# Performance work log

Measured on AMD Instinct MI355X. Metric: run time of the kernel, lower is better.

Reference implementation:

```python
import jax, jax.numpy as jnp
import numpy as np

T, B, IN, H, OUT, K = 1024, 128, 32, 512, 32, 64


def frac_weights(d):
    # d: [H] per-channel fractional differencing order (= 0.5*sigmoid(b_d)).
    # pi_j = pi_{j-1} * (j-1-d)/j, pi_0 = 1 (coeffs of (1-B)^d expansion).
    # Returned layout matches torch get_ws: index 0 -> lag K, index K-1 -> lag 1.
    j = jnp.arange(1, K + 1, dtype=d.dtype)[:, None]          # [K,1]
    pi = jnp.cumprod((j - 1.0 - d[None, :]) / j, axis=0)       # [K,H], pi[j-1]=coeff lag j
    return pi[::-1]                                            # [K,H]


def frac_filter(x, pi):
    # x: [T,B,H]; pi: [K,H] (lag K..1). Computes x_tilde[t] = x[t] + sum_j pi_j x[t-j]
    # (zero history before t=0, matching a zero-initialized memory buffer)
    # via a causal depthwise convolution.
    Hc = pi.shape[1]
    kern = jnp.concatenate([pi, jnp.ones((1, Hc), pi.dtype)], axis=0)  # [K+1,H]
    kern = kern.T[:, None, :]                                          # [H,1,K+1]
    xb = x.transpose(1, 2, 0)                                          # [B,H,T]
    y = jax.lax.conv_general_dilated(
        xb, kern, window_strides=(1,), padding=[(K, 0)],
        dimension_numbers=("NCH", "OIH", "NCH"), feature_group_count=Hc)
    return y.transpose(2, 0, 1)                                        # [T,B,H]


def rnn_layer(x, W_ih, b_ih, W_hh, b_hh, W_ho, b_ho, pi):
    # MRNNFixDCell over full sequence: fractional-differencing filter on the
    # layer input, then tanh RNN recurrence, then linear readout per step.
    xt = frac_filter(x, pi)
    pre = jnp.einsum('tbi,hi->tbh', xt, W_ih) + b_ih + b_hh   # input part precomputed

    def step(h, p):
        h = jnp.tanh(p + h @ W_hh.T)
        return h, h

    h0 = jnp.zeros((x.shape[1], W_hh.shape[0]), x.dtype)
    _, hs = jax.lax.scan(step, h0, pre)                        # [T,B,H]
    return jnp.einsum('tbh,oh->tbo', hs, W_ho) + b_ho          # [T,B,out]


def setup_inputs() -> dict:
    key = jax.random.key(0)
    ks = jax.random.split(key, 10)
    s = 0.05
    return {
        "inputs": jax.random.normal(ks[0], (T, B, IN), jnp.float32),
        "b_d":   jax.random.normal(ks[1], (1, H), jnp.float32) * 0.1,
        "W_emb": jax.random.normal(ks[2], (H, IN), jnp.float32) * s,
        "b_emb": jnp.zeros((H,), jnp.float32),
        "W_ih0": jax.random.normal(ks[3], (H, H), jnp.float32) * s,
        "b_ih0": jnp.zeros((H,), jnp.float32),
        "W_hh0": jax.random.normal(ks[4], (H, H), jnp.float32) * s,
        "b_hh0": jnp.zeros((H,), jnp.float32),
        "W_ho0": jax.random.normal(ks[5], (H, H), jnp.float32) * s,
        "b_ho0": jnp.zeros((H,), jnp.float32),
        "W_ih1": jax.random.normal(ks[6], (H, H), jnp.float32) * s,
        "b_ih1": jnp.zeros((H,), jnp.float32),
        "W_hh1": jax.random.normal(ks[7], (H, H), jnp.float32) * s,
        "b_hh1": jnp.zeros((H,), jnp.float32),
        "W_ho1": jax.random.normal(ks[8], (OUT, H), jnp.float32) * s,
        "b_ho1": jnp.zeros((OUT,), jnp.float32),
    }


def reference(inputs, b_d, W_emb, b_emb,
              W_ih0, b_ih0, W_hh0, b_hh0, W_ho0, b_ho0,
              W_ih1, b_ih1, W_hh1, b_hh1, W_ho1, b_ho1):
    x = jnp.einsum('tbi,hi->tbh', inputs, W_emb) + b_emb       # input embedding
    d = 0.5 * jax.nn.sigmoid(b_d)[0]                           # [H], fixed d per channel
    pi = frac_weights(d)                                       # [K,H]
    y0 = rnn_layer(x,  W_ih0, b_ih0, W_hh0, b_hh0, W_ho0, b_ho0, pi)
    y1 = rnn_layer(y0, W_ih1, b_ih1, W_hh1, b_hh1, W_ho1, b_ho1, pi)
    return y1[-1]                                              # last-step output [B,OUT]
```

## Files before the change

### kernel.cpp

```cpp
#include <hip/hip_runtime.h>
#include <hip/hip_bf16.h>

#define Tn 1024
#define Bn 128
#define INn 32
#define Hn 512
#define OUTn 32
#define Kn 64
#define LPAD 536

typedef __attribute__((ext_vector_type(8))) __bf16 bf16x8;
typedef __attribute__((ext_vector_type(4))) float f32x4;
typedef __attribute__((ext_vector_type(4))) unsigned int u32x4;
typedef __attribute__((ext_vector_type(2))) unsigned int u32x2;

typedef const __attribute__((address_space(1))) void* gas_p;
typedef __attribute__((address_space(3))) void* las_p;

static __device__ __forceinline__ float bf2f(unsigned short u) {
    union { unsigned int i; float f; } c; c.i = ((unsigned int)u) << 16; return c.f;
}
static __device__ __forceinline__ unsigned short f2bf(float f) {
    union { float f; unsigned int i; } c; c.f = f;
    unsigned int x = c.i;
    return (unsigned short)((x + 0x7fffu + ((x >> 16) & 1u)) >> 16);
}
static __device__ __forceinline__ float tanh_fast(float x) {
    float xc = fminf(fmaxf(x, -10.f), 10.f);
    float e = __expf(2.f * xc);
    return (e - 1.f) * __builtin_amdgcn_rcpf(e + 1.f);
}

__global__ __launch_bounds__(256) void cvt_k(const float* __restrict__ in,
                                             unsigned short* __restrict__ out, int n4) {
    int i = blockIdx.x * 256 + threadIdx.x;
    if (i < n4) {
        float4 v = ((const float4*)in)[i];
        ushort4 o;
        o.x = f2bf(v.x); o.y = f2bf(v.y); o.z = f2bf(v.z); o.w = f2bf(v.w);
        ((ushort4*)out)[i] = o;
    }
}

__global__ __launch_bounds__(512) void prep_small(const float* __restrict__ b_d,
                                                  const float* __restrict__ bih0, const float* __restrict__ bhh0,
                                                  const float* __restrict__ bih1, const float* __restrict__ bhh1,
                                                  float* __restrict__ pi, float* __restrict__ bias0,
                                                  float* __restrict__ bias1) {
    int i = threadIdx.x;
    float d = 0.5f / (1.0f + expf(-b_d[i]));
    float c = 1.0f;
    for (int j = 1; j <= Kn; ++j) {
        c *= ((float)(j - 1) - d) / (float)j;
        pi[(j - 1) * Hn + i] = c;
    }
    bias0[i] = bih0[i] + bhh0[i];
    bias1[i] = bih1[i] + bhh1[i];
}

__global__ __launch_bounds__(256, 2) void gemm_bt(const unsigned short* __restrict__ A,
                                                  const unsigned short* __restrict__ Bm,
                                                  unsigned short* __restrict__ C,
                                                  const float* __restrict__ bias,
                                                  int M, int N, int K) {
    __shared__ unsigned short As[128 * 32];
    __shared__ unsigned short Bs[128 * 32];
    int ntile = N >> 7;
    int bm = blockIdx.x / ntile;
    int bn = blockIdx.x - bm * ntile;
    size_t m0 = (size_t)bm << 7;
    int n0 = bn << 7;
    int tid = threadIdx.x;
    int lane = tid & 63, w = tid >> 6;
    int wm = w >> 1, wn = w & 1;
    int r = lane & 15, g = lane >> 4;
    int srow = tid >> 2, sblk = tid & 3;
    f32x4 acc[4][4] = {};
    for (int k0 = 0; k0 < K; k0 += 32) {
#pragma unroll
        for (int it = 0; it < 2; ++it) {
            const unsigned short* ga = A + (m0 + it * 64 + srow) * (size_t)K + k0 + sblk * 8;
            __builtin_amdgcn_global_load_lds((gas_p)ga, (las_p)((char*)As + it * 4096 + w * 1024), 16, 0, 0);
            const unsigned short* gbp = Bm + ((size_t)(n0 + it * 64 + srow)) * (size_t)K + k0 + sblk * 8;
            __builtin_amdgcn_global_load_lds((gas_p)gbp, (las_p)((char*)Bs + it * 4096 + w * 1024), 16, 0, 0);
        }
        __syncthreads();
        bf16x8 af[4], bfr[4];
#pragma unroll
        for (int m = 0; m < 4; ++m) af[m] = *(const bf16x8*)&As[(wm * 64 + m * 16 + r) * 32 + g * 8];
#pragma unroll
        for (int n = 0; n < 4; ++n) bfr[n] = *(const bf16x8*)&Bs[(wn * 64 + n * 16 + r) * 32 + g * 8];
#pragma unroll
        for (int m = 0; m < 4; ++m)
#pragma unroll
            for (int n = 0; n < 4; ++n)
                acc[m][n] = __builtin_amdgcn_mfma_f32_16x16x32_bf16(af[m], bfr[n], acc[m][n], 0, 0, 0);
        __syncthreads();
    }
#pragma unroll
    for (int n = 0; n < 4; ++n) {
        int col = n0 + wn * 64 + n * 16 + r;
        float bv = bias[col];
#pragma unroll
        for (int m = 0; m < 4; ++m) {
            size_t row0 = m0 + wm * 64 + m * 16 + g * 4;
#pragma unroll
            for (int q = 0; q < 4; ++q)
                C[(row0 + q) * (size_t)N + col] = f2bf(acc[m][n][q] + bv);
        }
    }
}

__global__ __launch_bounds__(256, 2) void filt_k(const unsigned short* __restrict__ X,
                                                 const float* __restrict__ Pi,
                                                 unsigned short* __restrict__ Y, int t_off) {
    int tid = threadIdx.x;
    int il = tid & 63, ts = tid >> 6;
    int i = blockIdx.x * 64 + il;
    int b = blockIdx.z;
    int tbase = t_off + blockIdx.y * 128 + ts * 32;
    float xr[96];
#pragma unroll
    for (int k2 = 0; k2 < 96; ++k2) {
        int t = tbase - 64 + k2;
        xr[k2] = (t >= 0) ? bf2f(X[(size_t)t * (Bn * Hn) + b * Hn + i]) : 0.0f;
    }
    float acc[32];
#pragma unroll
    for (int tt = 0; tt < 32; ++tt) acc[tt] = xr[64 + tt];
#pragma unroll
    for (int j = 1; j <= 64; ++j) {
        float p = Pi[(j - 1) * Hn + i];
#pragma unroll
        for (int tt = 0; tt < 32; ++tt) acc[tt] += p * xr[64 + tt - j];
    }
#pragma unroll
    for (int tt = 0; tt < 32; ++tt)
        Y[(size_t)(tbase - t_off + tt) * (Bn * Hn) + b * Hn + i] = f2bf(acc[tt]);
}

#define MFMA8(K0)                                                                              \
    {                                                                                          \
        _Pragma("unroll") for (int kk = 0; kk < 8; ++kk) {                                     \
            bf16x8 bf = *(const bf16x8*)(hrow + (K0 + kk) * 32 + g * 8);                       \
            acc0 = __builtin_amdgcn_mfma_f32_16x16x32_bf16(wreg0[K0 + kk], bf, acc0, 0, 0, 0); \
            acc1 = __builtin_amdgcn_mfma_f32_16x16x32_bf16(wreg1[K0 + kk], bf, acc1, 0, 0, 0); \
        }                                                                                      \
    }

__global__ __launch_bounds__(512, 2) void rec7_k(const unsigned short* __restrict__ W,
                                                 const unsigned short* pre,
                                                 unsigned short* hs,
                                                 float* __restrict__ hfin,
                                                 unsigned int* ex, int fbase) {
    __shared__ unsigned short hl[2][16][LPAD];
    int bid = blockIdx.x;
    int gb = bid & 7, go = bid >> 3;
    int tid = threadIdx.x, lane = tid & 63, w = tid >> 6;
    int r = lane & 15, g = lane >> 4;
    int ob = go * 256 + w * 32;
    bf16x8 wreg0[16], wreg1[16];
#pragma unroll
    for (int kk = 0; kk < 16; ++kk) {
        wreg0[kk] = *(const bf16x8*)(W + (size_t)(ob + r) * Hn + kk * 32 + g * 8);
        wreg1[kk] = *(const bf16x8*)(W + (size_t)(ob + 16 + r) * Hn + kk * 32 + g * 8);
    }
    int bb = gb * 16 + r;
    const unsigned short* preP = pre + (size_t)bb * Hn + ob + g * 4;
    unsigned short* hsP = hs ? hs + (size_t)bb * Hn + ob + g * 4 : (unsigned short*)0;
    int myblk = gb * 2 + go, pblk = gb * 2 + (go ^ 1);
    int pbatch = tid >> 5;
    int pcol = (go ^ 1) * 256 + (tid & 31) * 8;
    unsigned long long pfA0 = *(const unsigned long long*)(preP);
    unsigned long long pfA1 = *(const unsigned long long*)(preP + 16);
    unsigned long long pfB0 = *(const unsigned long long*)(preP + (size_t)(Bn * Hn));
    unsigned long long pfB1 = *(const unsigned long long*)(preP + (size_t)(Bn * Hn) + 16);

#define REC_STEP(TT, P0, P1, ISLAST)                                                             \
    {                                                                                            \
        asm volatile("s_waitcnt lgkmcnt(0)\n\ts_barrier" ::: "memory");   \
        f32x4 acc0 = {0.f, 0.f, 0.f, 0.f}, acc1 = {0.f, 0.f, 0.f, 0.f};                          \
        const unsigned short* hrow = &hl[TT & 1][r][0];                                          \
        if (TT > 0) {                                                                            \
            if (go == 0) MFMA8(0) else MFMA8(8)                           \
            unsigned tg = (unsigned)(fbase + TT);                                                \
            const unsigned int* pp = ex + ((size_t)(TT & 1) * 16 + pblk) * 4096 + tid * 8;       \
            u32x4 a, b;                                                                          \
            while (1) {                                                                          \
                asm volatile("global_load_dwordx4 %0, %2, off sc1\n\t"                           \
                             "global_load_dwordx4 %1, %2, off offset:16 sc1\n\t"                 \
                             "s_waitcnt vmcnt(0)"                                                \
                             : "=v"(a), "=v"(b) : "v"(pp) : "memory");                           \
                bool ok = (a.x & 0xffffu) == tg && (a.y & 0xffffu) == tg &&                      \
                          (a.z & 0xffffu) == tg && (a.w & 0xffffu) == tg &&                      \
                          (b.x & 0xffffu) == tg && (b.y & 0xffffu) == tg &&                      \
                          (b.z & 0xffffu) == tg && (b.w & 0xffffu) == tg;                        \
                if (ok) break;                                                                   \
            }                                                                                    \
            unsigned int* ld = (unsigned int*)&hl[TT & 1][pbatch][pcol];                         \
            ld[0] = (a.x >> 16) | (a.y & 0xffff0000u);                                           \
            ld[1] = (a.z >> 16) | (a.w & 0xffff0000u);                                           \
            ld[2] = (b.x >> 16) | (b.y & 0xffff0000u);                                           \
            ld[3] = (b.z >> 16) | (b.w & 0xffff0000u);                                           \
        }                                                                                        \
                \
        int tn = (TT + 2 < Tn) ? TT + 2 : Tn - 1;                                                \
        unsigned long long n0 = *(const unsigned long long*)(preP + (size_t)tn * (Bn * Hn));     \
        unsigned long long n1 = *(const unsigned long long*)(preP + (size_t)tn * (Bn * Hn) + 16);\
        asm volatile("s_waitcnt lgkmcnt(0)\n\ts_barrier" ::: "memory");    \
        if (TT > 0) {                                                                            \
            if (go == 0) MFMA8(8) else MFMA8(0)                       \
        }                                                                                        \
        union { unsigned long long u; unsigned short s[4]; } p0, p1;                             \
        p0.u = P0; p1.u = P1;                                                                    \
        float h0 = tanh_fast(acc0[0] + bf2f(p0.s[0]));                                           \
        float h1 = tanh_fast(acc0[1] + bf2f(p0.s[1]));                                           \
        float h2 = tanh_fast(acc0[2] + bf2f(p0.s[2]));                                           \
        float h3 = tanh_fast(acc0[3] + bf2f(p0.s[3]));                                           \
        float h4 = tanh_fast(acc1[0] + bf2f(p1.s[0]));                                           \
        float h5 = tanh_fast(acc1[1] + bf2f(p1.s[1]));                                           \
        float h6 = tanh_fast(acc1[2] + bf2f(p1.s[2]));                                           \
        float h7 = tanh_fast(acc1[3] + bf2f(p1.s[3]));                                           \
        unsigned int b0 = f2bf(h0), b1 = f2bf(h1), b2 = f2bf(h2), b3 = f2bf(h3);                 \
        unsigned int b4 = f2bf(h4), b5 = f2bf(h5), b6 = f2bf(h6), b7 = f2bf(h7);                 \
        unsigned tv = (unsigned)(fbase + TT + 1);                                                \
        u32x4 s0 = { (b0 << 16) | tv, (b1 << 16) | tv, (b2 << 16) | tv, (b3 << 16) | tv };       \
        u32x4 s1 = { (b4 << 16) | tv, (b5 << 16) | tv, (b6 << 16) | tv, (b7 << 16) | tv };       \
        unsigned int* wp = ex + ((size_t)((TT + 1) & 1) * 16 + myblk) * 4096 + r * 256 + w * 32 + g * 4; \
        asm volatile("global_store_dwordx4 %0, %1, off sc1\n\t"                                  \
                     "global_store_dwordx4 %0, %2, off offset:64 sc1"                            \
                     :: "v"(wp), "v"(s0), "v"(s1) : "memory");                                   \
        {                                                                                        \
            u32x2 v0 = { b0 | (b1 << 16), b2 | (b3 << 16) };                                     \
            u32x2 v1 = { b4 | (b5 << 16), b6 | (b7 << 16) };                                     \
            *(u32x2*)&hl[(TT + 1) & 1][r][ob + g * 4] = v0;                                      \
            *(u32x2*)&hl[(TT + 1) & 1][r][ob + 16 + g * 4] = v1;                                 \
        }                                                                                        \
        if (hsP) {                                                                               \
            union { unsigned int u[2]; unsigned long long v; } o0, o1;                           \
            o0.u[0] = b0 | (b1 << 16); o0.u[1] = b2 | (b3 << 16);                                \
            o1.u[0] = b4 | (b5 << 16); o1.u[1] = b6 | (b7 << 16);                                \
            *(unsigned long long*)(hsP + (size_t)TT * (Bn * Hn)) = o0.v;                         \
            *(unsigned long long*)(hsP + (size_t)TT * (Bn * Hn) + 16) = o1.v;                    \
        }                                                                                        \
        if (ISLAST && hfin) {                                                                    \
            float* hf = hfin + (size_t)bb * Hn + ob + g * 4;                                     \
            hf[0] = h0; hf[1] = h1; hf[2] = h2; hf[3] = h3;                                      \
            hf[16] = h4; hf[17] = h5; hf[18] = h6; hf[19] = h7;                                  \
        }                                                                                        \
        P0 = n0; P1 = n1;                                                                        \
    }

    for (int t = 0; t < Tn; t += 2) {
        REC_STEP(t, pfA0, pfA1, false)
        REC_STEP((t + 1), pfB0, pfB1, (t + 1 == Tn - 1))
    }
#undef REC_STEP
}

__global__ __launch_bounds__(64) void readout_k(const float* __restrict__ hfin,
                                                const float* __restrict__ Who1,
                                                const float* __restrict__ bho1,
                                                float* __restrict__ out) {
    int b = blockIdx.x;
    __shared__ float hv[Hn];
    int tid = threadIdx.x;
    for (int i = tid; i < Hn; i += 64) hv[i] = hfin[(size_t)b * Hn + i];
    __syncthreads();
    if (tid < OUTn) {
        float acc = bho1[tid];
        const float* wrow = Who1 + (size_t)tid * Hn;
#pragma unroll 8
        for (int i = 0; i < Hn; ++i) acc += wrow[i] * hv[i];
        out[b * OUTn + tid] = acc;
    }
}

extern "C" void kernel_launch(void* const* d_in, const int* in_sizes, int n_in,
                              void* d_out, int out_size, void* d_ws, size_t ws_size,
                              hipStream_t stream) {
    const float* inputs = (const float*)d_in[0];
    const float* b_d    = (const float*)d_in[1];
    const float* W_emb  = (const float*)d_in[2];
    const float* b_emb  = (const float*)d_in[3];
    const float* W_ih0  = (const float*)d_in[4];
    const float* b_ih0  = (const float*)d_in[5];
    const float* W_hh0  = (const float*)d_in[6];
    const float* b_hh0  = (const float*)d_in[7];
    const float* W_ho0  = (const float*)d_in[8];
    const float* b_ho0  = (const float*)d_in[9];
    const float* W_ih1  = (const float*)d_in[10];
    const float* b_ih1  = (const float*)d_in[11];
    const float* W_hh1  = (const float*)d_in[12];
    const float* b_hh1  = (const float*)d_in[13];
    const float* W_ho1  = (const float*)d_in[14];
    const float* b_ho1  = (const float*)d_in[15];

    char* ws = (char*)d_ws;
    size_t off = 0;
    auto alloc = [&](size_t bytes) {
        void* p = ws + off;
        off += (bytes + 255) & ~(size_t)255;
        return p;
    };
    unsigned short* B    = (unsigned short*)alloc(134217728);
    unsigned short* Hf   = (unsigned short*)alloc(67108864);
    unsigned short* inb  = (unsigned short*)alloc(8388608);
    unsigned short* Wemb = (unsigned short*)alloc(32768);
    unsigned short* Wih0 = (unsigned short*)alloc(524288);
    unsigned short* Whh0 = (unsigned short*)alloc(524288);
    unsigned short* Who0 = (unsigned short*)alloc(524288);
    unsigned short* Wih1 = (unsigned short*)alloc(524288);
    unsigned short* Whh1 = (unsigned short*)alloc(524288);
    float* bias0 = (float*)alloc(2048);
    float* bias1 = (float*)alloc(2048);
    float* piB   = (float*)alloc(131072);
    unsigned int* ex = (unsigned int*)alloc(524288);
    float* hfin = (float*)alloc(262144);
    (void)ws_size; (void)in_sizes; (void)n_in; (void)out_size;

    unsigned short* B_hi = B + (size_t)512 * Bn * Hn;
    const size_t halfBytes = 67108864;
    const int Mh = 512 * Bn;

    hipMemsetAsync(ex, 0, 524288, stream);
    cvt_k<<<4096, 256, 0, stream>>>(inputs, inb, 1048576);
    cvt_k<<<16,   256, 0, stream>>>(W_emb, Wemb, 4096);
    cvt_k<<<256,  256, 0, stream>>>(W_ih0, Wih0, 65536);
    cvt_k<<<256,  256, 0, stream>>>(W_hh0, Whh0, 65536);
    cvt_k<<<256,  256, 0, stream>>>(W_ho0, Who0, 65536);
    cvt_k<<<256,  256, 0, stream>>>(W_ih1, Wih1, 65536);
    cvt_k<<<256,  256, 0, stream>>>(W_hh1, Whh1, 65536);
    prep_small<<<1, 512, 0, stream>>>(b_d, b_ih0, b_hh0, b_ih1, b_hh1, piB, bias0, bias1);

    gemm_bt<<<4096, 256, 0, stream>>>(inb, Wemb, B, b_emb, Tn * Bn, Hn, INn);
    filt_k<<<dim3(8, 4, 128), 256, 0, stream>>>(B, piB, Hf, 512);
    gemm_bt<<<2048, 256, 0, stream>>>(Hf, Wih0, B_hi, bias0, Mh, Hn, Hn);
    filt_k<<<dim3(8, 4, 128), 256, 0, stream>>>(B, piB, Hf, 0);
    gemm_bt<<<2048, 256, 0, stream>>>(Hf, Wih0, B, bias0, Mh, Hn, Hn);
    rec7_k<<<16, 512, 0, stream>>>(Whh0, B, B, nullptr, ex, 0);
    gemm_bt<<<2048, 256, 0, stream>>>(B_hi, Who0, Hf, b_ho0, Mh, Hn, Hn);
    hipMemcpyAsync(B_hi, Hf, halfBytes, hipMemcpyDeviceToDevice, stream);
    gemm_bt<<<2048, 256, 0, stream>>>(B, Who0, Hf, b_ho0, Mh, Hn, Hn);
    hipMemcpyAsync(B, Hf, halfBytes, hipMemcpyDeviceToDevice, stream);
    filt_k<<<dim3(8, 4, 128), 256, 0, stream>>>(B, piB, Hf, 512);
    gemm_bt<<<2048, 256, 0, stream>>>(Hf, Wih1, B_hi, bias1, Mh, Hn, Hn);
    filt_k<<<dim3(8, 4, 128), 256, 0, stream>>>(B, piB, Hf, 0);
    gemm_bt<<<2048, 256, 0, stream>>>(Hf, Wih1, B, bias1, Mh, Hn, Hn);
    rec7_k<<<16, 512, 0, stream>>>(Whh1, B, nullptr, hfin, ex, 1024);
    readout_k<<<128, 64, 0, stream>>>(hfin, W_ho1, b_ho1, (float*)d_out);
}
```

Measured before the change: 5.597 ms.

## Halve recurrence block width, issue exchange loads before barrier, deepen prefetch

The recurrent kernel now uses 256 threads per block, with each wave computing 64 output rows through four MFMA accumulators and holding 64 bf16x8 weight registers. The cross-block exchange loads are issued before the first barrier so their latency overlaps the local MFMA half, and polling backs off with s_sleep. The pre-activation prefetch is deepened to four steps. The intent is to cut per-step barrier and synchronisation latency on the serial critical path, at the cost of heavy register pressure and fewer waves to hide latency.

```diff
diff --git a/kernel.cpp b/kernel.cpp
--- a/kernel.cpp
+++ b/kernel.cpp
@@ -139,123 +139,174 @@
         Y[(size_t)(tbase - t_off + tt) * (Bn * Hn) + b * Hn + i] = f2bf(acc[tt]);
 }
 
-#define MFMA8(K0)                                                                              \
-    {                                                                                          \
-        _Pragma("unroll") for (int kk = 0; kk < 8; ++kk) {                                     \
-            bf16x8 bf = *(const bf16x8*)(hrow + (K0 + kk) * 32 + g * 8);                       \
-            acc0 = __builtin_amdgcn_mfma_f32_16x16x32_bf16(wreg0[K0 + kk], bf, acc0, 0, 0, 0); \
-            acc1 = __builtin_amdgcn_mfma_f32_16x16x32_bf16(wreg1[K0 + kk], bf, acc1, 0, 0, 0); \
-        }                                                                                      \
-    }
-
-__global__ __launch_bounds__(512, 2) void rec7_k(const unsigned short* __restrict__ W,
-                                                 const unsigned short* pre,
-                                                 unsigned short* hs,
-                                                 float* __restrict__ hfin,
-                                                 unsigned int* ex, int fbase) {
+__global__ __launch_bounds__(256, 1) void rec10_k(const unsigned short* __restrict__ W,
+                                                  const unsigned short* pre,
+                                                  unsigned short* hs,
+                                                  float* __restrict__ hfin,
+                                                  unsigned int* ex, int fbase) {
     __shared__ unsigned short hl[2][16][LPAD];
     int bid = blockIdx.x;
     int gb = bid & 7, go = bid >> 3;
     int tid = threadIdx.x, lane = tid & 63, w = tid >> 6;
     int r = lane & 15, g = lane >> 4;
-    int ob = go * 256 + w * 32;
-    bf16x8 wreg0[16], wreg1[16];
-#pragma unroll
-    for (int kk = 0; kk < 16; ++kk) {
-        wreg0[kk] = *(const bf16x8*)(W + (size_t)(ob + r) * Hn + kk * 32 + g * 8);
-        wreg1[kk] = *(const bf16x8*)(W + (size_t)(ob + 16 + r) * Hn + kk * 32 + g * 8);
-    }
+    int ob = go * 256 + w * 64;
+    bf16x8 wreg[4][16];
+#pragma unroll
+    for (int m = 0; m < 4; ++m)
+#pragma unroll
+        for (int kk = 0; kk < 16; ++kk)
+            wreg[m][kk] = *(const bf16x8*)(W + (size_t)(ob + m * 16 + r) * Hn + kk * 32 + g * 8);
     int bb = gb * 16 + r;
     const unsigned short* preP = pre + (size_t)bb * Hn + ob + g * 4;
     unsigned short* hsP = hs ? hs + (size_t)bb * Hn + ob + g * 4 : (unsigned short*)0;
     int myblk = gb * 2 + go, pblk = gb * 2 + (go ^ 1);
-    int pbatch = tid >> 5;
-    int pcol = (go ^ 1) * 256 + (tid & 31) * 8;
-    unsigned long long pfA0 = *(const unsigned long long*)(preP);
-    unsigned long long pfA1 = *(const unsigned long long*)(preP + 16);
-    unsigned long long pfB0 = *(const unsigned long long*)(preP + (size_t)(Bn * Hn));
-    unsigned long long pfB1 = *(const unsigned long long*)(preP + (size_t)(Bn * Hn) + 16);
-
-#define REC_STEP(TT, P0, P1, ISLAST)                                                             \
+    int pb = tid >> 4;
+    int po = (tid & 15) * 16;
+    unsigned long long pfA0, pfA1, pfA2, pfA3, pfB0, pfB1, pfB2, pfB3;
+    unsigned long long pfC0, pfC1, pfC2, pfC3, pfD0, pfD1, pfD2, pfD3;
+#define LD4(S0, S1, S2, S3, TI)                                                              \
+    S0 = *(const unsigned long long*)(preP + (size_t)(TI) * (Bn * Hn));                      \
+    S1 = *(const unsigned long long*)(preP + (size_t)(TI) * (Bn * Hn) + 16);                 \
+    S2 = *(const unsigned long long*)(preP + (size_t)(TI) * (Bn * Hn) + 32);                 \
+    S3 = *(const unsigned long long*)(preP + (size_t)(TI) * (Bn * Hn) + 48);
+    LD4(pfA0, pfA1, pfA2, pfA3, 0)
+    LD4(pfB0, pfB1, pfB2, pfB3, 1)
+    LD4(pfC0, pfC1, pfC2, pfC3, 2)
+    LD4(pfD0, pfD1, pfD2, pfD3, 3)
+
+#define CHK4(V) ((V.x & 0xffffu) == tg && (V.y & 0xffffu) == tg && \
+                 (V.z & 0xffffu) == tg && (V.w & 0xffffu) == tg)
+#define MFMA_RANGE(K0)                                                                       \
+    {                                                                                        \
+        _Pragma("unroll") for (int kk = K0; kk < K0 + 8; ++kk) {                             \
+            bf16x8 hb = *(const bf16x8*)&hl[p][r][kk * 32 + g * 8];                          \
+            acc0 = __builtin_amdgcn_mfma_f32_16x16x32_bf16(wreg[0][kk], hb, acc0, 0, 0, 0);  \
+            acc1 = __builtin_amdgcn_mfma_f32_16x16x32_bf16(wreg[1][kk], hb, acc1, 0, 0, 0);  \
+            acc2 = __builtin_amdgcn_mfma_f32_16x16x32_bf16(wreg[2][kk], hb, acc2, 0, 0, 0);  \
+            acc3 = __builtin_amdgcn_mfma_f32_16x16x32_bf16(wreg[3][kk], hb, acc3, 0, 0, 0);  \
+        }                                                                                    \
+    }
+
+#define REC_STEP(TT, P0, P1, P2, P3, ISLAST)                                                     \
     {                                                                                            \
-        asm volatile("s_waitcnt lgkmcnt(0)\n\ts_barrier" ::: "memory");   \
+        const int p = TT & 1;                                                                    \
+        u32x4 a0, a1, a2, a3;                                                                    \
+        const unsigned int* pp = ex + ((size_t)p * 16 + pblk) * 4096 + pb * 256 + po;            \
+        unsigned tg = (unsigned)(fbase + TT);                                                    \
+        if (TT > 0) {                                                                            \
+            asm volatile("global_load_dwordx4 %0, %4, off sc1\n\t"                               \
+                         "global_load_dwordx4 %1, %4, off offset:16 sc1\n\t"                     \
+                         "global_load_dwordx4 %2, %4, off offset:32 sc1\n\t"                     \
+                         "global_load_dwordx4 %3, %4, off offset:48 sc1"                         \
+                         : "=v"(a0), "=v"(a1), "=v"(a2), "=v"(a3) : "v"(pp) : "memory");         \
+        }                                                                                        \
+        asm volatile("s_waitcnt lgkmcnt(0)\n\ts_barrier" ::: "memory");      \
         f32x4 acc0 = {0.f, 0.f, 0.f, 0.f}, acc1 = {0.f, 0.f, 0.f, 0.f};                          \
-        const unsigned short* hrow = &hl[TT & 1][r][0];                                          \
+        f32x4 acc2 = {0.f, 0.f, 0.f, 0.f}, acc3 = {0.f, 0.f, 0.f, 0.f};                          \
         if (TT > 0) {                                                                            \
-            if (go == 0) MFMA8(0) else MFMA8(8)                           \
-            unsigned tg = (unsigned)(fbase + TT);                                                \
-            const unsigned int* pp = ex + ((size_t)(TT & 1) * 16 + pblk) * 4096 + tid * 8;       \
-            u32x4 a, b;                                                                          \
-            while (1) {                                                                          \
-                asm volatile("global_load_dwordx4 %0, %2, off sc1\n\t"                           \
-                             "global_load_dwordx4 %1, %2, off offset:16 sc1\n\t"                 \
+            if (go == 0) MFMA_RANGE(0) else MFMA_RANGE(8)       \
+            asm volatile("s_waitcnt vmcnt(0)"                                                    \
+                         : "+v"(a0), "+v"(a1), "+v"(a2), "+v"(a3) :: "memory");                  \
+            while (!(CHK4(a0) && CHK4(a1) && CHK4(a2) && CHK4(a3))) {                            \
+                __builtin_amdgcn_s_sleep(1);                                                     \
+                asm volatile("global_load_dwordx4 %0, %4, off sc1\n\t"                           \
+                             "global_load_dwordx4 %1, %4, off offset:16 sc1\n\t"                 \
+                             "global_load_dwordx4 %2, %4, off offset:32 sc1\n\t"                 \
+                             "global_load_dwordx4 %3, %4, off offset:48 sc1\n\t"                 \
                              "s_waitcnt vmcnt(0)"                                                \
-                             : "=v"(a), "=v"(b) : "v"(pp) : "memory");                           \
-                bool ok = (a.x & 0xffffu) == tg && (a.y & 0xffffu) == tg &&                      \
-                          (a.z & 0xffffu) == tg && (a.w & 0xffffu) == tg &&                      \
-                          (b.x & 0xffffu) == tg && (b.y & 0xffffu) == tg &&                      \
-                          (b.z & 0xffffu) == tg && (b.w & 0xffffu) == tg;                        \
-                if (ok) break;                                                                   \
+                             : "=v"(a0), "=v"(a1), "=v"(a2), "=v"(a3) : "v"(pp) : "memory");     \
             }                                                                                    \
-            unsigned int* ld = (unsigned int*)&hl[TT & 1][pbatch][pcol];                         \
-            ld[0] = (a.x >> 16) | (a.y & 0xffff0000u);                                           \
-            ld[1] = (a.z >> 16) | (a.w & 0xffff0000u);                                           \
-            ld[2] = (b.x >> 16) | (b.y & 0xffff0000u);                                           \
-            ld[3] = (b.z >> 16) | (b.w & 0xffff0000u);                                           \
-        }                                                                                        \
-                \
-        int tn = (TT + 2 < Tn) ? TT + 2 : Tn - 1;                                                \
-        unsigned long long n0 = *(const unsigned long long*)(preP + (size_t)tn * (Bn * Hn));     \
-        unsigned long long n1 = *(const unsigned long long*)(preP + (size_t)tn * (Bn * Hn) + 16);\
+            unsigned int d0 = (a0.x >> 16) | (a0.y & 0xffff0000u);                               \
+            unsigned int d1 = (a0.z >> 16) | (a0.w & 0xffff0000u);                               \
+            unsigned int d2 = (a1.x >> 16) | (a1.y & 0xffff0000u);                               \
+            unsigned int d3 = (a1.z >> 16) | (a1.w & 0xffff0000u);                               \
+            unsigned int d4 = (a2.x >> 16) | (a2.y & 0xffff0000u);                               \
+            unsigned int d5 = (a2.z >> 16) | (a2.w & 0xffff0000u);                               \
+            unsigned int d6 = (a3.x >> 16) | (a3.y & 0xffff0000u);                               \
+            unsigned int d7 = (a3.z >> 16) | (a3.w & 0xffff0000u);                               \
+            unsigned short* sd = &hl[p][pb][(go ^ 1) * 256 + po];                                \
+            u32x4 w0 = { d0, d1, d2, d3 }, w1 = { d4, d5, d6, d7 };                              \
+            *(u32x4*)sd = w0; *(u32x4*)(sd + 8) = w1;                                            \
+        }                                                                                        \
         asm volatile("s_waitcnt lgkmcnt(0)\n\ts_barrier" ::: "memory");    \
         if (TT > 0) {                                                                            \
-            if (go == 0) MFMA8(8) else MFMA8(0)                       \
-        }                                                                                        \
-        union { unsigned long long u; unsigned short s[4]; } p0, p1;                             \
-        p0.u = P0; p1.u = P1;                                                                    \
-        float h0 = tanh_fast(acc0[0] + bf2f(p0.s[0]));                                           \
-        float h1 = tanh_fast(acc0[1] + bf2f(p0.s[1]));                                           \
-        float h2 = tanh_fast(acc0[2] + bf2f(p0.s[2]));                                           \
-        float h3 = tanh_fast(acc0[3] + bf2f(p0.s[3]));                                           \
-        float h4 = tanh_fast(acc1[0] + bf2f(p1.s[0]));                                           \
-        float h5 = tanh_fast(acc1[1] + bf2f(p1.s[1]));                                           \
-        float h6 = tanh_fast(acc1[2] + bf2f(p1.s[2]));                                           \
-        float h7 = tanh_fast(acc1[3] + bf2f(p1.s[3]));                                           \
-        unsigned int b0 = f2bf(h0), b1 = f2bf(h1), b2 = f2bf(h2), b3 = f2bf(h3);                 \
-        unsigned int b4 = f2bf(h4), b5 = f2bf(h5), b6 = f2bf(h6), b7 = f2bf(h7);                 \
+            if (go == 0) MFMA_RANGE(8) else MFMA_RANGE(0)                                        \
+        }                                                                                        \
+        union { unsigned long long u; unsigned short s[4]; } q0, q1, q2, q3;                     \
+        q0.u = P0; q1.u = P1; q2.u = P2; q3.u = P3;                                              \
+        float hv0 = tanh_fast(acc0[0] + bf2f(q0.s[0]));                                          \
+        float hv1 = tanh_fast(acc0[1] + bf2f(q0.s[1]));                                          \
+        float hv2 = tanh_fast(acc0[2] + bf2f(q0.s[2]));                                          \
+        float hv3 = tanh_fast(acc0[3] + bf2f(q0.s[3]));                                          \
+        float hv4 = tanh_fast(acc1[0] + bf2f(q1.s[0]));                                          \
+        float hv5 = tanh_fast(acc1[1] + bf2f(q1.s[1]));                                          \
+        float hv6 = tanh_fast(acc1[2] + bf2f(q1.s[2]));                                          \
+        float hv7 = tanh_fast(acc1[3] + bf2f(q1.s[3]));                                          \
+        float hv8 = tanh_fast(acc2[0] + bf2f(q2.s[0]));                                          \
+        float hv9 = tanh_fast(acc2[1] + bf2f(q2.s[1]));                                          \
+        float hva = tanh_fast(acc2[2] + bf2f(q2.s[2]));                                          \
+        float hvb = tanh_fast(acc2[3] + bf2f(q2.s[3]));                                          \
+        float hvc = tanh_fast(acc3[0] + bf2f(q3.s[0]));                                          \
+        float hvd = tanh_fast(acc3[1] + bf2f(q3.s[1]));                                          \
+        float hve = tanh_fast(acc3[2] + bf2f(q3.s[2]));                                          \
+        float hvf = tanh_fast(acc3[3] + bf2f(q3.s[3]));                                          \
+        unsigned int b0 = f2bf(hv0), b1 = f2bf(hv1), b2 = f2bf(hv2), b3 = f2bf(hv3);             \
+        unsigned int b4 = f2bf(hv4), b5 = f2bf(hv5), b6 = f2bf(hv6), b7 = f2bf(hv7);             \
+        unsigned int b8 = f2bf(hv8), b9 = f2bf(hv9), ba = f2bf(hva), bc2 = f2bf(hvb);            \
+        unsigned int bc = f2bf(hvc), bd = f2bf(hvd), be = f2bf(hve), bf_ = f2bf(hvf);            \
         unsigned tv = (unsigned)(fbase + TT + 1);                                                \
         u32x4 s0 = { (b0 << 16) | tv, (b1 << 16) | tv, (b2 << 16) | tv, (b3 << 16) | tv };       \
         u32x4 s1 = { (b4 << 16) | tv, (b5 << 16) | tv, (b6 << 16) | tv, (b7 << 16) | tv };       \
-        unsigned int* wp = ex + ((size_t)((TT + 1) & 1) * 16 + myblk) * 4096 + r * 256 + w * 32 + g * 4; \
+        u32x4 s2 = { (b8 << 16) | tv, (b9 << 16) | tv, (ba << 16) | tv, (bc2 << 16) | tv };      \
+        u32x4 s3 = { (bc << 16) | tv, (bd << 16) | tv, (be << 16) | tv, (bf_ << 16) | tv };      \
+        unsigned int* wp = ex + ((size_t)((TT + 1) & 1) * 16 + myblk) * 4096 + r * 256 + w * 64 + g * 4; \
         asm volatile("global_store_dwordx4 %0, %1, off sc1\n\t"                                  \
-                     "global_store_dwordx4 %0, %2, off offset:64 sc1"                            \
-                     :: "v"(wp), "v"(s0), "v"(s1) : "memory");                                   \
+                     "global_store_dwordx4 %0, %2, off offset:64 sc1\n\t"                        \
+                     "global_store_dwordx4 %0, %3, off offset:128 sc1\n\t"                       \
+                     "global_store_dwordx4 %0, %4, off offset:192 sc1"                           \
+                     :: "v"(wp), "v"(s0), "v"(s1), "v"(s2), "v"(s3) : "memory");                 \
         {                                                                                        \
             u32x2 v0 = { b0 | (b1 << 16), b2 | (b3 << 16) };                                     \
             u32x2 v1 = { b4 | (b5 << 16), b6 | (b7 << 16) };                                     \
-            *(u32x2*)&hl[(TT + 1) & 1][r][ob + g * 4] = v0;                                      \
-            *(u32x2*)&hl[(TT + 1) & 1][r][ob + 16 + g * 4] = v1;                                 \
+            u32x2 v2 = { b8 | (b9 << 16), ba | (bc2 << 16) };                                    \
+            u32x2 v3 = { bc | (bd << 16), be | (bf_ << 16) };                                    \
+            *(u32x2*)&hl[p ^ 1][r][ob + g * 4]      = v0;                                        \
+            *(u32x2*)&hl[p ^ 1][r][ob + 16 + g * 4] = v1;                                        \
+            *(u32x2*)&hl[p ^ 1][r][ob + 32 + g * 4] = v2;                                        \
+            *(u32x2*)&hl[p ^ 1][r][ob + 48 + g * 4] = v3;                                        \
         }                                                                                        \
         if (hsP) {                                                                               \
-            union { unsigned int u[2]; unsigned long long v; } o0, o1;                           \
+            union { unsigned int u[2]; unsigned long long v; } o0, o1, o2, o3;                   \
             o0.u[0] = b0 | (b1 << 16); o0.u[1] = b2 | (b3 << 16);                                \
             o1.u[0] = b4 | (b5 << 16); o1.u[1] = b6 | (b7 << 16);                                \
-            *(unsigned long long*)(hsP + (size_t)TT * (Bn * Hn)) = o0.v;                         \
+            o2.u[0] = b8 | (b9 << 16); o2.u[1] = ba | (bc2 << 16);                               \
+            o3.u[0] = bc | (bd << 16); o3.u[1] = be | (bf_ << 16);                               \
+            *(unsigned long long*)(hsP + (size_t)TT * (Bn * Hn))      = o0.v;                    \
             *(unsigned long long*)(hsP + (size_t)TT * (Bn * Hn) + 16) = o1.v;                    \
+            *(unsigned long long*)(hsP + (size_t)TT * (Bn * Hn) + 32) = o2.v;                    \
+            *(unsigned long long*)(hsP + (size_t)TT * (Bn * Hn) + 48) = o3.v;                    \
         }                                                                                        \
         if (ISLAST && hfin) {                                                                    \
             float* hf = hfin + (size_t)bb * Hn + ob + g * 4;                                     \
-            hf[0] = h0; hf[1] = h1; hf[2] = h2; hf[3] = h3;                                      \
-            hf[16] = h4; hf[17] = h5; hf[18] = h6; hf[19] = h7;                                  \
-        }                                                                                        \
-        P0 = n0; P1 = n1;                                                                        \
-    }
-
-    for (int t = 0; t < Tn; t += 2) {
-        REC_STEP(t, pfA0, pfA1, false)
-        REC_STEP((t + 1), pfB0, pfB1, (t + 1 == Tn - 1))
+            hf[0]  = hv0; hf[1]  = hv1; hf[2]  = hv2; hf[3]  = hv3;                              \
+            hf[16] = hv4; hf[17] = hv5; hf[18] = hv6; hf[19] = hv7;                              \
+            hf[32] = hv8; hf[33] = hv9; hf[34] = hva; hf[35] = hvb;                              \
+            hf[48] = hvc; hf[49] = hvd; hf[50] = hve; hf[51] = hvf;                              \
+        }                                                                                        \
+        int tn = (TT + 4 < Tn) ? TT + 4 : Tn - 1;                       \
+        LD4(P0, P1, P2, P3, tn)                                                                  \
+    }
+
+    for (int t = 0; t < Tn; t += 4) {
+        REC_STEP(t,       pfA0, pfA1, pfA2, pfA3, false)
+        REC_STEP((t + 1), pfB0, pfB1, pfB2, pfB3, false)
+        REC_STEP((t + 2), pfC0, pfC1, pfC2, pfC3, false)
+        REC_STEP((t + 3), pfD0, pfD1, pfD2, pfD3, (t + 3 == Tn - 1))
     }
 #undef REC_STEP
+#undef MFMA_RANGE
+#undef CHK4
+#undef LD4
 }
 
 __global__ __launch_bounds__(64) void readout_k(const float* __restrict__ hfin,
@@ -338,7 +389,7 @@
     gemm_bt<<<2048, 256, 0, stream>>>(Hf, Wih0, B_hi, bias0, Mh, Hn, Hn);
     filt_k<<<dim3(8, 4, 128), 256, 0, stream>>>(B, piB, Hf, 0);
     gemm_bt<<<2048, 256, 0, stream>>>(Hf, Wih0, B, bias0, Mh, Hn, Hn);
-    rec7_k<<<16, 512, 0, stream>>>(Whh0, B, B, nullptr, ex, 0);
+    rec10_k<<<16, 256, 0, stream>>>(Whh0, B, B, nullptr, ex, 0);
     gemm_bt<<<2048, 256, 0, stream>>>(B_hi, Who0, Hf, b_ho0, Mh, Hn, Hn);
     hipMemcpyAsync(B_hi, Hf, halfBytes, hipMemcpyDeviceToDevice, stream);
     gemm_bt<<<2048, 256, 0, stream>>>(B, Who0, Hf, b_ho0, Mh, Hn, Hn);
@@ -347,6 +398,6 @@
     gemm_bt<<<2048, 256, 0, stream>>>(Hf, Wih1, B_hi, bias1, Mh, Hn, Hn);
     filt_k<<<dim3(8, 4, 128), 256, 0, stream>>>(B, piB, Hf, 0);
     gemm_bt<<<2048, 256, 0, stream>>>(Hf, Wih1, B, bias1, Mh, Hn, Hn);
-    rec7_k<<<16, 512, 0, stream>>>(Whh1, B, nullptr, hfin, ex, 1024);
+    rec10_k<<<16, 256, 0, stream>>>(Whh1, B, nullptr, hfin, ex, 1024);
     readout_k<<<128, 64, 0, stream>>>(hfin, W_ho1, b_ho1, (float*)d_out);
 }
```

Result: slower. 7.458 ms (+33.2%).

## Replace two-block cross-CU hidden-state exchange with single 1024-thread block per batch group

Applied to the files above, without the earlier changes.

The recurrence kernel previously split each 16-batch group's 512 output columns across two 512-thread blocks that exchanged the hidden state every step through global memory, using tagged spin-wait polling. Now one 1024-thread block owns all 512 columns, so the full hidden state stays in LDS and each step needs only a block barrier. This removes the global-memory handshake latency and the exchange buffer, but halves the grid to 8 blocks. Each thread still keeps 32 weight vectors in registers, so register pressure at 1024 threads per block is a risk.

```diff
diff --git a/kernel.cpp b/kernel.cpp
--- a/kernel.cpp
+++ b/kernel.cpp
@@ -11,7 +11,6 @@
 
 typedef __attribute__((ext_vector_type(8))) __bf16 bf16x8;
 typedef __attribute__((ext_vector_type(4))) float f32x4;
-typedef __attribute__((ext_vector_type(4))) unsigned int u32x4;
 typedef __attribute__((ext_vector_type(2))) unsigned int u32x2;
 
 typedef const __attribute__((address_space(1))) void* gas_p;
@@ -139,26 +138,15 @@
         Y[(size_t)(tbase - t_off + tt) * (Bn * Hn) + b * Hn + i] = f2bf(acc[tt]);
 }
 
-#define MFMA8(K0)                                                                              \
-    {                                                                                          \
-        _Pragma("unroll") for (int kk = 0; kk < 8; ++kk) {                                     \
-            bf16x8 bf = *(const bf16x8*)(hrow + (K0 + kk) * 32 + g * 8);                       \
-            acc0 = __builtin_amdgcn_mfma_f32_16x16x32_bf16(wreg0[K0 + kk], bf, acc0, 0, 0, 0); \
-            acc1 = __builtin_amdgcn_mfma_f32_16x16x32_bf16(wreg1[K0 + kk], bf, acc1, 0, 0, 0); \
-        }                                                                                      \
-    }
-
-__global__ __launch_bounds__(512, 2) void rec7_k(const unsigned short* __restrict__ W,
-                                                 const unsigned short* pre,
-                                                 unsigned short* hs,
-                                                 float* __restrict__ hfin,
-                                                 unsigned int* ex, int fbase) {
+__global__ __launch_bounds__(1024, 1) void rec12_k(const unsigned short* __restrict__ W,
+                                                   const unsigned short* pre,
+                                                   unsigned short* hs,
+                                                   float* __restrict__ hfin) {
     __shared__ unsigned short hl[2][16][LPAD];
-    int bid = blockIdx.x;
-    int gb = bid & 7, go = bid >> 3;
+    int gb = blockIdx.x;
     int tid = threadIdx.x, lane = tid & 63, w = tid >> 6;
     int r = lane & 15, g = lane >> 4;
-    int ob = go * 256 + w * 32;
+    int ob = w * 32;
     bf16x8 wreg0[16], wreg1[16];
 #pragma unroll
     for (int kk = 0; kk < 16; ++kk) {
@@ -168,9 +156,6 @@
     int bb = gb * 16 + r;
     const unsigned short* preP = pre + (size_t)bb * Hn + ob + g * 4;
     unsigned short* hsP = hs ? hs + (size_t)bb * Hn + ob + g * 4 : (unsigned short*)0;
-    int myblk = gb * 2 + go, pblk = gb * 2 + (go ^ 1);
-    int pbatch = tid >> 5;
-    int pcol = (go ^ 1) * 256 + (tid & 31) * 8;
     unsigned long long pfA0 = *(const unsigned long long*)(preP);
     unsigned long long pfA1 = *(const unsigned long long*)(preP + 16);
     unsigned long long pfB0 = *(const unsigned long long*)(preP + (size_t)(Bn * Hn));
@@ -178,63 +163,37 @@
 
 #define REC_STEP(TT, P0, P1, ISLAST)                                                             \
     {                                                                                            \
-        asm volatile("s_waitcnt lgkmcnt(0)\n\ts_barrier" ::: "memory");   \
+        const int p = TT & 1;                                                                    \
+        asm volatile("s_waitcnt lgkmcnt(0)\n\ts_barrier" ::: "memory");       \
         f32x4 acc0 = {0.f, 0.f, 0.f, 0.f}, acc1 = {0.f, 0.f, 0.f, 0.f};                          \
-        const unsigned short* hrow = &hl[TT & 1][r][0];                                          \
         if (TT > 0) {                                                                            \
-            if (go == 0) MFMA8(0) else MFMA8(8)                           \
-            unsigned tg = (unsigned)(fbase + TT);                                                \
-            const unsigned int* pp = ex + ((size_t)(TT & 1) * 16 + pblk) * 4096 + tid * 8;       \
-            u32x4 a, b;                                                                          \
-            while (1) {                                                                          \
-                asm volatile("global_load_dwordx4 %0, %2, off sc1\n\t"                           \
-                             "global_load_dwordx4 %1, %2, off offset:16 sc1\n\t"                 \
-                             "s_waitcnt vmcnt(0)"                                                \
-                             : "=v"(a), "=v"(b) : "v"(pp) : "memory");                           \
-                bool ok = (a.x & 0xffffu) == tg && (a.y & 0xffffu) == tg &&                      \
-                          (a.z & 0xffffu) == tg && (a.w & 0xffffu) == tg &&                      \
-                          (b.x & 0xffffu) == tg && (b.y & 0xffffu) == tg &&                      \
-                          (b.z & 0xffffu) == tg && (b.w & 0xffffu) == tg;                        \
-                if (ok) break;                                                                   \
+            _Pragma("unroll") for (int kk = 0; kk < 16; ++kk) {                                  \
+                bf16x8 hb = *(const bf16x8*)&hl[p][r][kk * 32 + g * 8];                          \
+                acc0 = __builtin_amdgcn_mfma_f32_16x16x32_bf16(wreg0[kk], hb, acc0, 0, 0, 0);    \
+                acc1 = __builtin_amdgcn_mfma_f32_16x16x32_bf16(wreg1[kk], hb, acc1, 0, 0, 0);    \
             }                                                                                    \
-            unsigned int* ld = (unsigned int*)&hl[TT & 1][pbatch][pcol];                         \
-            ld[0] = (a.x >> 16) | (a.y & 0xffff0000u);                                           \
-            ld[1] = (a.z >> 16) | (a.w & 0xffff0000u);                                           \
-            ld[2] = (b.x >> 16) | (b.y & 0xffff0000u);                                           \
-            ld[3] = (b.z >> 16) | (b.w & 0xffff0000u);                                           \
         }                                                                                        \
-                \
+                                \
         int tn = (TT + 2 < Tn) ? TT + 2 : Tn - 1;                                                \
         unsigned long long n0 = *(const unsigned long long*)(preP + (size_t)tn * (Bn * Hn));     \
         unsigned long long n1 = *(const unsigned long long*)(preP + (size_t)tn * (Bn * Hn) + 16);\
-        asm volatile("s_waitcnt lgkmcnt(0)\n\ts_barrier" ::: "memory");    \
-        if (TT > 0) {                                                                            \
-            if (go == 0) MFMA8(8) else MFMA8(0)                       \
-        }                                                                                        \
-        union { unsigned long long u; unsigned short s[4]; } p0, p1;                             \
-        p0.u = P0; p1.u = P1;                                                                    \
-        float h0 = tanh_fast(acc0[0] + bf2f(p0.s[0]));                                           \
-        float h1 = tanh_fast(acc0[1] + bf2f(p0.s[1]));                                           \
-        float h2 = tanh_fast(acc0[2] + bf2f(p0.s[2]));                                           \
-        float h3 = tanh_fast(acc0[3] + bf2f(p0.s[3]));                                           \
-        float h4 = tanh_fast(acc1[0] + bf2f(p1.s[0]));                                           \
-        float h5 = tanh_fast(acc1[1] + bf2f(p1.s[1]));                                           \
-        float h6 = tanh_fast(acc1[2] + bf2f(p1.s[2]));                                           \
-        float h7 = tanh_fast(acc1[3] + bf2f(p1.s[3]));                                           \
+        union { unsigned long long u; unsigned short s[4]; } q0, q1;                             \
+        q0.u = P0; q1.u = P1;                                                                    \
+        float h0 = tanh_fast(acc0[0] + bf2f(q0.s[0]));                                           \
+        float h1 = tanh_fast(acc0[1] + bf2f(q0.s[1]));                                           \
+        float h2 = tanh_fast(acc0[2] + bf2f(q0.s[2]));                                           \
+        float h3 = tanh_fast(acc0[3] + bf2f(q0.s[3]));                                           \
+        float h4 = tanh_fast(acc1[0] + bf2f(q1.s[0]));                                           \
+        float h5 = tanh_fast(acc1[1] + bf2f(q1.s[1]));                                           \
+        float h6 = tanh_fast(acc1[2] + bf2f(q1.s[2]));                                           \
+        float h7 = tanh_fast(acc1[3] + bf2f(q1.s[3]));                                           \
         unsigned int b0 = f2bf(h0), b1 = f2bf(h1), b2 = f2bf(h2), b3 = f2bf(h3);                 \
         unsigned int b4 = f2bf(h4), b5 = f2bf(h5), b6 = f2bf(h6), b7 = f2bf(h7);                 \
-        unsigned tv = (unsigned)(fbase + TT + 1);                                                \
-        u32x4 s0 = { (b0 << 16) | tv, (b1 << 16) | tv, (b2 << 16) | tv, (b3 << 16) | tv };       \
-        u32x4 s1 = { (b4 << 16) | tv, (b5 << 16) | tv, (b6 << 16) | tv, (b7 << 16) | tv };       \
-        unsigned int* wp = ex + ((size_t)((TT + 1) & 1) * 16 + myblk) * 4096 + r * 256 + w * 32 + g * 4; \
-        asm volatile("global_store_dwordx4 %0, %1, off sc1\n\t"                                  \
-                     "global_store_dwordx4 %0, %2, off offset:64 sc1"                            \
-                     :: "v"(wp), "v"(s0), "v"(s1) : "memory");                                   \
         {                                                                                        \
             u32x2 v0 = { b0 | (b1 << 16), b2 | (b3 << 16) };                                     \
             u32x2 v1 = { b4 | (b5 << 16), b6 | (b7 << 16) };                                     \
-            *(u32x2*)&hl[(TT + 1) & 1][r][ob + g * 4] = v0;                                      \
-            *(u32x2*)&hl[(TT + 1) & 1][r][ob + 16 + g * 4] = v1;                                 \
+            *(u32x2*)&hl[p ^ 1][r][ob + g * 4] = v0;                                             \
+            *(u32x2*)&hl[p ^ 1][r][ob + 16 + g * 4] = v1;                                        \
         }                                                                                        \
         if (hsP) {                                                                               \
             union { unsigned int u[2]; unsigned long long v; } o0, o1;                           \
@@ -315,15 +274,13 @@
     float* bias0 = (float*)alloc(2048);
     float* bias1 = (float*)alloc(2048);
     float* piB   = (float*)alloc(131072);
-    unsigned int* ex = (unsigned int*)alloc(524288);
-    float* hfin = (float*)alloc(262144);
+    float* hfin  = (float*)alloc(262144);
     (void)ws_size; (void)in_sizes; (void)n_in; (void)out_size;
 
     unsigned short* B_hi = B + (size_t)512 * Bn * Hn;
     const size_t halfBytes = 67108864;
     const int Mh = 512 * Bn;
 
-    hipMemsetAsync(ex, 0, 524288, stream);
     cvt_k<<<4096, 256, 0, stream>>>(inputs, inb, 1048576);
     cvt_k<<<16,   256, 0, stream>>>(W_emb, Wemb, 4096);
     cvt_k<<<256,  256, 0, stream>>>(W_ih0, Wih0, 65536);
@@ -338,7 +295,7 @@
     gemm_bt<<<2048, 256, 0, stream>>>(Hf, Wih0, B_hi, bias0, Mh, Hn, Hn);
     filt_k<<<dim3(8, 4, 128), 256, 0, stream>>>(B, piB, Hf, 0);
     gemm_bt<<<2048, 256, 0, stream>>>(Hf, Wih0, B, bias0, Mh, Hn, Hn);
-    rec7_k<<<16, 512, 0, stream>>>(Whh0, B, B, nullptr, ex, 0);
+    rec12_k<<<8, 1024, 0, stream>>>(Whh0, B, B, nullptr);
     gemm_bt<<<2048, 256, 0, stream>>>(B_hi, Who0, Hf, b_ho0, Mh, Hn, Hn);
     hipMemcpyAsync(B_hi, Hf, halfBytes, hipMemcpyDeviceToDevice, stream);
     gemm_bt<<<2048, 256, 0, stream>>>(B, Who0, Hf, b_ho0, Mh, Hn, Hn);
@@ -347,6 +304,6 @@
     gemm_bt<<<2048, 256, 0, stream>>>(Hf, Wih1, B_hi, bias1, Mh, Hn, Hn);
     filt_k<<<dim3(8, 4, 128), 256, 0, stream>>>(B, piB, Hf, 0);
     gemm_bt<<<2048, 256, 0, stream>>>(Hf, Wih1, B, bias1, Mh, Hn, Hn);
-    rec7_k<<<16, 512, 0, stream>>>(Whh1, B, nullptr, hfin, ex, 1024);
+    rec12_k<<<8, 1024, 0, stream>>>(Whh1, B, nullptr, hfin);
     readout_k<<<128, 64, 0, stream>>>(hfin, W_ho1, b_ho1, (float*)d_out);
 }
```

New measurement: 12.56 ms. 124% more time.
